# Kernel tuning notes

Measured on AMD Instinct MI355X. Metric: run time of the kernel, lower is better.

## Reference

```python
import jax, jax.numpy as jnp
import numpy as np

N_NODES = 20000
N_EDGES = 200000
D = 64            # node_encoding
H = 4             # num_heads
GRAPH_LAYERS = 2
FLOW_ITERS = 10


def seg_softmax(logits, seg, n):
    # numerically stable softmax over segments (per-row softmax of sparse matrix)
    m = jax.ops.segment_max(logits, seg, num_segments=n)
    e = jnp.exp(logits - m[seg])
    s = jax.ops.segment_sum(e, seg, num_segments=n)
    return e / s[seg]


def setup_inputs() -> dict:
    key = jax.random.key(0)
    ks = jax.random.split(key, 12)
    sc = 1.0 / np.sqrt(D)
    return {
        "node_embeddings": jax.random.normal(ks[0], (N_NODES, D), jnp.float32),
        "demands": jax.random.normal(ks[1], (N_NODES, 1), jnp.float32),
        "edge_row": jax.random.randint(ks[2], (N_EDGES,), 0, N_NODES, jnp.int32),
        "edge_col": jax.random.randint(ks[3], (N_EDGES,), 0, N_NODES, jnp.int32),
        "W_gat": jax.random.normal(ks[4], (H, D, D), jnp.float32) * sc,
        "a_src": jax.random.normal(ks[5], (H, D), jnp.float32) * sc,
        "a_dst": jax.random.normal(ks[6], (H, D), jnp.float32) * sc,
        "Wx": jax.random.normal(ks[7], (D, 3 * D), jnp.float32) * sc,
        "Wh": jax.random.normal(ks[8], (D, 3 * D), jnp.float32) * sc,
        "b_gru": jnp.zeros((3 * D,), jnp.float32),
        "Wd": jax.random.normal(ks[9], (D + 1, 1), jnp.float32) * sc,
        "bd": jnp.zeros((1,), jnp.float32),
    }


def reference(node_embeddings, demands, edge_row, edge_col,
              W_gat, a_src, a_dst, Wx, Wh, b_gru, Wd, bd):
    n = node_embeddings.shape[0]
    h = node_embeddings

    for _ in range(GRAPH_LAYERS):
        # ---- SparseGAT over adjacency edge list ----
        f = jnp.einsum('nd,hde->hne', h, W_gat)          # [H,N,D] per-head features
        s_src = jnp.einsum('hne,he->hn', f, a_src)       # [H,N]
        s_dst = jnp.einsum('hne,he->hn', f, a_dst)       # [H,N]
        logits = jax.nn.leaky_relu(s_src[:, edge_row] + s_dst[:, edge_col], 0.2)  # [H,E]
        alpha = jax.vmap(lambda l: seg_softmax(l, edge_row, n))(logits)           # [H,E]
        msgs = alpha[:, :, None] * f[:, edge_col, :]                              # [H,E,D]
        agg = jax.vmap(lambda m: jax.ops.segment_sum(m, edge_row, num_segments=n))(msgs)  # [H,N,D]
        gat_out = agg.mean(axis=0)                       # average heads -> [N,D]

        # ---- GRU node update (relu candidate activation), state = h ----
        xg = gat_out @ Wx + b_gru                        # [N,3D]
        z = jax.nn.sigmoid(xg[:, :D] + h @ Wh[:, :D])
        r = jax.nn.sigmoid(xg[:, D:2 * D] + h @ Wh[:, D:2 * D])
        hh = jax.nn.relu(xg[:, 2 * D:] + (r * h) @ Wh[:, 2 * D:])
        h = z * h + (1.0 - z) * hh

    # ---- decoder: linear over concat(encoding, demands) ----
    pred_w = jnp.concatenate([h, demands], axis=1) @ Wd + bd   # [N,1]

    # ---- sparse softmax of (adj * pred_weights) per source row ----
    w = seg_softmax(pred_w[edge_row, 0], edge_row, n)          # [E]

    # ---- iterative sparse MCF flow solve ----
    d_pos = jax.nn.relu(demands[:, 0])                         # source injections

    def step(flow, _):
        inflow = d_pos + jax.ops.segment_sum(flow, edge_col, num_segments=n)
        return w * inflow[edge_row], None

    flow, _ = jax.lax.scan(step, jnp.zeros_like(w), None, length=FLOW_ITERS)
    return flow
```

## Files before the change

### kernel.cpp

```cpp
#include <hip/hip_runtime.h>


#define N_NODES 20000
#define N_EDGES 200000
#define FLOW_ITERS 10
#define NBLK 128
#define NTHR 512
#define NPB 157
#define CAP 24
#define NQUAD 50000
#define QPB 391
#define OFL_MAX 4096
#define NP1 (N_NODES + 1)

__device__ __forceinline__ float ld_coh(const float* p) {
    return __hip_atomic_load(p, __ATOMIC_RELAXED, __HIP_MEMORY_SCOPE_AGENT);
}
__device__ __forceinline__ int ld_coh_i(const int* p) {
    return __hip_atomic_load(p, __ATOMIC_RELAXED, __HIP_MEMORY_SCOPE_AGENT);
}
__device__ __forceinline__ void st_coh(float* p, float v) {
    __hip_atomic_store(p, v, __ATOMIC_RELAXED, __HIP_MEMORY_SCOPE_AGENT);
}
__device__ __forceinline__ void st_coh_i(int* p, int v) {
    __hip_atomic_store(p, v, __ATOMIC_RELAXED, __HIP_MEMORY_SCOPE_AGENT);
}

__device__ __forceinline__ void gbar(int* grp, int ord) {
    __syncthreads();
    if (threadIdx.x == 0) {
        __hip_atomic_fetch_add(&grp[(blockIdx.x & 7) * 32], 1,
                               __ATOMIC_RELAXED, __HIP_MEMORY_SCOPE_AGENT);
        const int target = NBLK * ord;
        for (;;) {
            int s = 0;
            #pragma unroll
            for (int g = 0; g < 8; ++g)
                s += __hip_atomic_load(&grp[g * 32], __ATOMIC_RELAXED,
                                       __HIP_MEMORY_SCOPE_AGENT);
            if (s >= target) break;
            __builtin_amdgcn_s_sleep(1);
        }
    }
    __syncthreads();
}

__global__ __launch_bounds__(NTHR)
void mcf_fused(const float* __restrict__ demands,
               const int* __restrict__ edge_row,
               const int* __restrict__ edge_col,
               float* __restrict__ out,
               int* __restrict__ deg,
               int* __restrict__ fill,
               float* __restrict__ V0,
               float* __restrict__ V1b,
               int* __restrict__ pcsc,
               int* __restrict__ ofl_cnt,
               int* __restrict__ ofl_v,
               int* __restrict__ ofl_row,
               int* __restrict__ grp)
{
    const int tx = threadIdx.x, bx = blockIdx.x;
    int bar = 0;

    __shared__ float part[NTHR];

    const int m = bx * QPB + tx;
    const bool bld = (tx < QPB) && (m < NQUAD);
    int4 r4 = {0, 0, 0, 0}, c4 = {0, 0, 0, 0};
    if (bld) {
        r4 = ((const int4*)edge_row)[m];
        c4 = ((const int4*)edge_col)[m];
        int rr[4] = {r4.x, r4.y, r4.z, r4.w};
        int cc[4] = {c4.x, c4.y, c4.z, c4.w};
        #pragma unroll
        for (int i = 0; i < 4; ++i) {
            __hip_atomic_fetch_add(&deg[rr[i]], 1, __ATOMIC_RELAXED, __HIP_MEMORY_SCOPE_AGENT);
            int idx = __hip_atomic_fetch_add(&fill[cc[i]], 1,
                                             __ATOMIC_RELAXED, __HIP_MEMORY_SCOPE_AGENT);
            if (idx < CAP) {
                st_coh_i(&pcsc[cc[i] * CAP + idx], rr[i]);
            } else {
                int o = __hip_atomic_fetch_add(ofl_cnt, 1,
                                               __ATOMIC_RELAXED, __HIP_MEMORY_SCOPE_AGENT);
                if (o < OFL_MAX) { st_coh_i(&ofl_v[o], cc[i]); st_coh_i(&ofl_row[o], rr[i]); }
            }
        }
    }
    gbar(grp, ++bar);

    const int g = tx / 3, q = tx - 3 * g;
    const int v = bx * NPB + g;
    const bool active = (g < NPB) && (v < N_NODES);
    float dposv = 0.0f, invd = 0.0f;
    int   cnt = 0, ocnt = 0;
    int   er[8];
    if (active) {
        cnt = min(ld_coh_i(&fill[v]), CAP);
        const int4* pb = (const int4*)&pcsc[v * CAP + q * 8];
        int4 a = pb[0], b = pb[1];
        er[0]=a.x; er[1]=a.y; er[2]=a.z; er[3]=a.w;
        er[4]=b.x; er[5]=b.y; er[6]=b.z; er[7]=b.w;
        if (q == 0) {
            dposv  = fmaxf(demands[v], 0.0f);
            int dv = ld_coh_i(&deg[v]);
            invd   = (dv > 0) ? (1.0f / (float)dv) : 0.0f;
            ocnt   = ld_coh_i(ofl_cnt);
            st_coh(&V0[v], dposv * invd);
        }
    }
    gbar(grp, ++bar);

    #pragma unroll 1
    for (int j = 2; j <= FLOW_ITERS; ++j) {
        const float* Vp = (j & 1) ? V1b : V0;
        float*       Vn = (j & 1) ? V0 : V1b;
        if (active) {
            float p = 0.0f;
            #pragma unroll
            for (int s = 0; s < 8; ++s)
                if (q * 8 + s < cnt) p += ld_coh(&Vp[er[s]]);
            part[tx] = p;
        }
        __syncthreads();
        if (active && q == 0) {
            float acc = dposv + part[tx] + part[tx + 1] + part[tx + 2];
            if (ocnt > 0) {
                for (int o = 0; o < ocnt && o < OFL_MAX; ++o)
                    if (ld_coh_i(&ofl_v[o]) == v)
                        acc += ld_coh(&Vp[ld_coh_i(&ofl_row[o])]);
            }
            st_coh(&Vn[v], acc * invd);
        }
        gbar(grp, ++bar);
    }

    if (bld) {
        float4 o4;
        o4.x = ld_coh(&V1b[r4.x]);
        o4.y = ld_coh(&V1b[r4.y]);
        o4.z = ld_coh(&V1b[r4.z]);
        o4.w = ld_coh(&V1b[r4.w]);
        ((float4*)out)[m] = o4;
    }
}

extern "C" void kernel_launch(void* const* d_in, const int* in_sizes, int n_in,
                              void* d_out, int out_size, void* d_ws, size_t ws_size,
                              hipStream_t stream) {
    const float* demands  = (const float*)d_in[1];
    const int*   edge_row = (const int*)d_in[2];
    const int*   edge_col = (const int*)d_in[3];
    float*       out      = (float*)d_out;

    char* ws = (char*)d_ws;
    auto take = [&](size_t bytes) {
        void* p = (void*)ws;
        ws += (bytes + 127) & ~size_t(127);
        return p;
    };
    char* zone0 = ws;
    int*   deg     = (int*)  take(N_NODES * 4);
    int*   fill    = (int*)  take(N_NODES * 4);
    float* V0      = (float*)take(NP1 * 4);
    float* V1b     = (float*)take(NP1 * 4);
    int*   ofl_cnt = (int*)  take(4);
    int*   grp     = (int*)  take(8 * 32 * 4);
    size_t zone0_bytes = (size_t)(ws - zone0);
    int*   pcsc    = (int*)  take((size_t)N_NODES * CAP * 4);
    int*   ofl_v   = (int*)  take(OFL_MAX * 4);
    int*   ofl_row = (int*)  take(OFL_MAX * 4);

    hipMemsetAsync(zone0, 0x00, zone0_bytes, stream);
    mcf_fused<<<NBLK, NTHR, 0, stream>>>(demands, edge_row, edge_col, out,
                                         deg, fill, V0, V1b, pcsc,
                                         ofl_cnt, ofl_v, ofl_row, grp);
}
```

Baseline: 122.4 us.

## Replace per-iteration grid barriers with NaN-sentinel dataflow across level buffers

Removes the grid-wide barrier after each flow iteration. Each iteration level now gets its own buffer, pre-filled with a NaN bit pattern by a memset, and each node spins on its in-neighbours' entries until they are written, so waiting is point-to-point. It also computes the first level directly from demands and degrees, which saves one barrier, and assigns one thread per node instead of three. Risks include spin livelock if producers are not co-resident, reduced per-node parallelism, an extra memset, and a valid result that happens to equal the sentinel bit pattern.

Result: slower. 141.3 us (+15.4%).

```diff
diff --git a/kernel.cpp b/kernel.cpp
--- a/kernel.cpp
+++ b/kernel.cpp
@@ -12,8 +12,14 @@
 #define QPB 391
 #define OFL_MAX 4096
 #define NP1 (N_NODES + 1)
+#define NLVL 9
+#define NANP 0xFFFFFFFFu
+#define SPIN_MAX 65536
 
 __device__ __forceinline__ float ld_coh(const float* p) {
+    return __hip_atomic_load(p, __ATOMIC_RELAXED, __HIP_MEMORY_SCOPE_AGENT);
+}
+__device__ __forceinline__ unsigned ld_coh_u(const unsigned* p) {
     return __hip_atomic_load(p, __ATOMIC_RELAXED, __HIP_MEMORY_SCOPE_AGENT);
 }
 __device__ __forceinline__ int ld_coh_i(const int* p) {
@@ -32,7 +38,7 @@
         __hip_atomic_fetch_add(&grp[(blockIdx.x & 7) * 32], 1,
                                __ATOMIC_RELAXED, __HIP_MEMORY_SCOPE_AGENT);
         const int target = NBLK * ord;
-        for (;;) {
+        for (int t = 0; t < SPIN_MAX; ++t) {
             int s = 0;
             #pragma unroll
             for (int g = 0; g < 8; ++g)
@@ -52,8 +58,7 @@
                float* __restrict__ out,
                int* __restrict__ deg,
                int* __restrict__ fill,
-               float* __restrict__ V0,
-               float* __restrict__ V1b,
+               float* __restrict__ W,
                int* __restrict__ pcsc,
                int* __restrict__ ofl_cnt,
                int* __restrict__ ofl_v,
@@ -62,8 +67,6 @@
 {
     const int tx = threadIdx.x, bx = blockIdx.x;
     int bar = 0;
-
-    __shared__ float part[NTHR];
 
     const int m = bx * QPB + tx;
     const bool bld = (tx < QPB) && (m < NQUAD);
@@ -89,58 +92,94 @@
     }
     gbar(grp, ++bar);
 
-    const int g = tx / 3, q = tx - 3 * g;
-    const int v = bx * NPB + g;
-    const bool active = (g < NPB) && (v < N_NODES);
-    float dposv = 0.0f, invd = 0.0f;
-    int   cnt = 0, ocnt = 0;
-    int   er[8];
-    if (active) {
-        cnt = min(ld_coh_i(&fill[v]), CAP);
-        const int4* pb = (const int4*)&pcsc[v * CAP + q * 8];
-        int4 a = pb[0], b = pb[1];
-        er[0]=a.x; er[1]=a.y; er[2]=a.z; er[3]=a.w;
-        er[4]=b.x; er[5]=b.y; er[6]=b.z; er[7]=b.w;
-        if (q == 0) {
-            dposv  = fmaxf(demands[v], 0.0f);
-            int dv = ld_coh_i(&deg[v]);
-            invd   = (dv > 0) ? (1.0f / (float)dv) : 0.0f;
-            ocnt   = ld_coh_i(ofl_cnt);
-            st_coh(&V0[v], dposv * invd);
-        }
-    }
-    gbar(grp, ++bar);
-
-    #pragma unroll 1
-    for (int j = 2; j <= FLOW_ITERS; ++j) {
-        const float* Vp = (j & 1) ? V1b : V0;
-        float*       Vn = (j & 1) ? V0 : V1b;
-        if (active) {
-            float p = 0.0f;
-            #pragma unroll
-            for (int s = 0; s < 8; ++s)
-                if (q * 8 + s < cnt) p += ld_coh(&Vp[er[s]]);
-            part[tx] = p;
-        }
-        __syncthreads();
-        if (active && q == 0) {
-            float acc = dposv + part[tx] + part[tx + 1] + part[tx + 2];
+    const int v = bx * NPB + tx;
+    const bool own = (tx < NPB) && (v < N_NODES);
+    if (own) {
+        const int cnt = min(ld_coh_i(&fill[v]), CAP);
+        int er[CAP];
+        {
+            const int4* pb = (const int4*)&pcsc[v * CAP];
+            #pragma unroll
+            for (int qq = 0; qq < 6; ++qq) {
+                int4 a = pb[qq];
+                er[qq * 4 + 0] = a.x; er[qq * 4 + 1] = a.y;
+                er[qq * 4 + 2] = a.z; er[qq * 4 + 3] = a.w;
+            }
+        }
+        const float dposv = fmaxf(demands[v], 0.0f);
+        const int   dv    = ld_coh_i(&deg[v]);
+        const float invd  = (dv > 0) ? (1.0f / (float)dv) : 0.0f;
+        const int   ocnt  = ld_coh_i(ofl_cnt);
+
+        {
+            float fd[CAP]; int gd[CAP];
+            #pragma unroll
+            for (int s = 0; s < CAP; ++s)
+                if (s < cnt) { fd[s] = demands[er[s]]; gd[s] = ld_coh_i(&deg[er[s]]); }
+            float acc = dposv;
+            #pragma unroll
+            for (int s = 0; s < CAP; ++s)
+                if (s < cnt) acc += fmaxf(fd[s], 0.0f) * (1.0f / (float)gd[s]);
             if (ocnt > 0) {
                 for (int o = 0; o < ocnt && o < OFL_MAX; ++o)
-                    if (ld_coh_i(&ofl_v[o]) == v)
-                        acc += ld_coh(&Vp[ld_coh_i(&ofl_row[o])]);
-            }
-            st_coh(&Vn[v], acc * invd);
-        }
-        gbar(grp, ++bar);
-    }
+                    if (ld_coh_i(&ofl_v[o]) == v) {
+                        int r = ld_coh_i(&ofl_row[o]);
+                        acc += fmaxf(demands[r], 0.0f)
+                             * (1.0f / (float)ld_coh_i(&deg[r]));
+                    }
+            }
+            st_coh(&W[v], acc * invd);
+        }
+
+        #pragma unroll 1
+        for (int k = 1; k < NLVL; ++k) {
+            const float* Wp = W + (size_t)(k - 1) * NP1;
+            unsigned uv[CAP];
+            unsigned pend = (unsigned)((1ull << cnt) - 1ull);
+            int guard = 0;
+            while (pend) {
+                #pragma unroll
+                for (int s = 0; s < CAP; ++s)
+                    if ((pend >> s) & 1u)
+                        uv[s] = ld_coh_u((const unsigned*)&Wp[er[s]]);
+                unsigned np = pend;
+                #pragma unroll
+                for (int s = 0; s < CAP; ++s)
+                    if (((pend >> s) & 1u) && uv[s] != NANP) np &= ~(1u << s);
+                pend = np;
+                if (pend) {
+                    if (++guard > SPIN_MAX) break;
+                    __builtin_amdgcn_s_sleep(2);
+                }
+            }
+            float acc = dposv;
+            #pragma unroll
+            for (int s = 0; s < CAP; ++s)
+                if (s < cnt) acc += __uint_as_float(uv[s]);
+            if (ocnt > 0) {
+                for (int o = 0; o < ocnt && o < OFL_MAX; ++o)
+                    if (ld_coh_i(&ofl_v[o]) == v) {
+                        int r = ld_coh_i(&ofl_row[o]);
+                        unsigned u = NANP;
+                        for (int t = 0; t < SPIN_MAX; ++t) {
+                            u = ld_coh_u((const unsigned*)&Wp[r]);
+                            if (u != NANP) break;
+                        }
+                        acc += __uint_as_float(u);
+                    }
+            }
+            st_coh(&W[(size_t)k * NP1 + v], acc * invd);
+        }
+    }
+    gbar(grp, ++bar);
 
     if (bld) {
+        const float* W9 = W + (size_t)(NLVL - 1) * NP1;
         float4 o4;
-        o4.x = ld_coh(&V1b[r4.x]);
-        o4.y = ld_coh(&V1b[r4.y]);
-        o4.z = ld_coh(&V1b[r4.z]);
-        o4.w = ld_coh(&V1b[r4.w]);
+        o4.x = ld_coh(&W9[r4.x]);
+        o4.y = ld_coh(&W9[r4.y]);
+        o4.z = ld_coh(&W9[r4.z]);
+        o4.w = ld_coh(&W9[r4.w]);
         ((float4*)out)[m] = o4;
     }
 }
@@ -162,17 +201,19 @@
     char* zone0 = ws;
     int*   deg     = (int*)  take(N_NODES * 4);
     int*   fill    = (int*)  take(N_NODES * 4);
-    float* V0      = (float*)take(NP1 * 4);
-    float* V1b     = (float*)take(NP1 * 4);
     int*   ofl_cnt = (int*)  take(4);
     int*   grp     = (int*)  take(8 * 32 * 4);
     size_t zone0_bytes = (size_t)(ws - zone0);
+    char* zoneF = ws;
+    float* W       = (float*)take((size_t)NLVL * NP1 * 4);
+    size_t zoneF_bytes = (size_t)(ws - zoneF);
     int*   pcsc    = (int*)  take((size_t)N_NODES * CAP * 4);
     int*   ofl_v   = (int*)  take(OFL_MAX * 4);
     int*   ofl_row = (int*)  take(OFL_MAX * 4);
 
     hipMemsetAsync(zone0, 0x00, zone0_bytes, stream);
+    hipMemsetAsync(zoneF, 0xFF, zoneF_bytes, stream);
     mcf_fused<<<NBLK, NTHR, 0, stream>>>(demands, edge_row, edge_col, out,
-                                         deg, fill, V0, V1b, pcsc,
+                                         deg, fill, W, pcsc,
                                          ofl_cnt, ofl_v, ofl_row, grp);
 }
```

## Split build into separate kernel and run flow with one node per thread

Applied to the files above, without the earlier changes.

Moves the CSC build into its own launch so the kernel boundary replaces one grid barrier. The flow kernel now runs on 40 blocks with one thread per node holding all 24 neighbour indices in registers, which removes the shared-memory partial reduction and lets each barrier wait on fewer blocks. It also computes the second iteration directly from demands and degrees, saving one barrier round. The tradeoffs are an extra launch, higher register pressure, fewer CUs doing the gather, and a bounded spin in the barrier that could break correctness if it ever times out.

New measurement: 147.5 us. +20.5%, slower.

```diff
diff --git a/kernel.cpp b/kernel.cpp
--- a/kernel.cpp
+++ b/kernel.cpp
@@ -3,26 +3,20 @@
 
 #define N_NODES 20000
 #define N_EDGES 200000
-#define FLOW_ITERS 10
-#define NBLK 128
 #define NTHR 512
-#define NPB 157
+#define NBLK1 128
+#define QPB 391
+#define NBLK2 40
 #define CAP 24
 #define NQUAD 50000
-#define QPB 391
 #define OFL_MAX 4096
 #define NP1 (N_NODES + 1)
+#define SPIN_MAX 65536
 
 __device__ __forceinline__ float ld_coh(const float* p) {
     return __hip_atomic_load(p, __ATOMIC_RELAXED, __HIP_MEMORY_SCOPE_AGENT);
 }
-__device__ __forceinline__ int ld_coh_i(const int* p) {
-    return __hip_atomic_load(p, __ATOMIC_RELAXED, __HIP_MEMORY_SCOPE_AGENT);
-}
 __device__ __forceinline__ void st_coh(float* p, float v) {
-    __hip_atomic_store(p, v, __ATOMIC_RELAXED, __HIP_MEMORY_SCOPE_AGENT);
-}
-__device__ __forceinline__ void st_coh_i(int* p, int v) {
     __hip_atomic_store(p, v, __ATOMIC_RELAXED, __HIP_MEMORY_SCOPE_AGENT);
 }
 
@@ -31,8 +25,8 @@
     if (threadIdx.x == 0) {
         __hip_atomic_fetch_add(&grp[(blockIdx.x & 7) * 32], 1,
                                __ATOMIC_RELAXED, __HIP_MEMORY_SCOPE_AGENT);
-        const int target = NBLK * ord;
-        for (;;) {
+        const int target = NBLK2 * ord;
+        for (int t = 0; t < SPIN_MAX; ++t) {
             int s = 0;
             #pragma unroll
             for (int g = 0; g < 8; ++g)
@@ -46,102 +40,126 @@
 }
 
 __global__ __launch_bounds__(NTHR)
-void mcf_fused(const float* __restrict__ demands,
-               const int* __restrict__ edge_row,
-               const int* __restrict__ edge_col,
-               float* __restrict__ out,
-               int* __restrict__ deg,
-               int* __restrict__ fill,
-               float* __restrict__ V0,
-               float* __restrict__ V1b,
-               int* __restrict__ pcsc,
-               int* __restrict__ ofl_cnt,
-               int* __restrict__ ofl_v,
-               int* __restrict__ ofl_row,
-               int* __restrict__ grp)
+void build_k(const int* __restrict__ edge_row,
+             const int* __restrict__ edge_col,
+             int* __restrict__ deg,
+             int* __restrict__ fill,
+             int* __restrict__ pcsc,
+             int* __restrict__ ofl_cnt,
+             int* __restrict__ ofl_v,
+             int* __restrict__ ofl_row)
+{
+    const int m = blockIdx.x * QPB + threadIdx.x;
+    if (threadIdx.x < QPB && m < NQUAD) {
+        int4 r4 = ((const int4*)edge_row)[m];
+        int4 c4 = ((const int4*)edge_col)[m];
+        int rr[4] = {r4.x, r4.y, r4.z, r4.w};
+        int cc[4] = {c4.x, c4.y, c4.z, c4.w};
+        #pragma unroll
+        for (int i = 0; i < 4; ++i) {
+            __hip_atomic_fetch_add(&deg[rr[i]], 1,
+                                   __ATOMIC_RELAXED, __HIP_MEMORY_SCOPE_AGENT);
+            int idx = __hip_atomic_fetch_add(&fill[cc[i]], 1,
+                                             __ATOMIC_RELAXED, __HIP_MEMORY_SCOPE_AGENT);
+            if (idx < CAP) {
+                pcsc[cc[i] * CAP + idx] = rr[i];
+            } else {
+                int o = __hip_atomic_fetch_add(ofl_cnt, 1,
+                                               __ATOMIC_RELAXED, __HIP_MEMORY_SCOPE_AGENT);
+                if (o < OFL_MAX) { ofl_v[o] = cc[i]; ofl_row[o] = rr[i]; }
+            }
+        }
+    }
+}
+
+__global__ __launch_bounds__(NTHR)
+void flow_k(const float* __restrict__ demands,
+            const int* __restrict__ edge_row,
+            float* __restrict__ out,
+            const int* __restrict__ deg,
+            const int* __restrict__ fill,
+            const int* __restrict__ pcsc,
+            const int* __restrict__ ofl_cnt,
+            const int* __restrict__ ofl_v,
+            const int* __restrict__ ofl_row,
+            float* __restrict__ V0,
+            float* __restrict__ V1b,
+            int* __restrict__ grp)
 {
     const int tx = threadIdx.x, bx = blockIdx.x;
     int bar = 0;
 
-    __shared__ float part[NTHR];
-
-    const int m = bx * QPB + tx;
-    const bool bld = (tx < QPB) && (m < NQUAD);
-    int4 r4 = {0, 0, 0, 0}, c4 = {0, 0, 0, 0};
-    if (bld) {
-        r4 = ((const int4*)edge_row)[m];
-        c4 = ((const int4*)edge_col)[m];
-        int rr[4] = {r4.x, r4.y, r4.z, r4.w};
-        int cc[4] = {c4.x, c4.y, c4.z, c4.w};
-        #pragma unroll
-        for (int i = 0; i < 4; ++i) {
-            __hip_atomic_fetch_add(&deg[rr[i]], 1, __ATOMIC_RELAXED, __HIP_MEMORY_SCOPE_AGENT);
-            int idx = __hip_atomic_fetch_add(&fill[cc[i]], 1,
-                                             __ATOMIC_RELAXED, __HIP_MEMORY_SCOPE_AGENT);
-            if (idx < CAP) {
-                st_coh_i(&pcsc[cc[i] * CAP + idx], rr[i]);
-            } else {
-                int o = __hip_atomic_fetch_add(ofl_cnt, 1,
-                                               __ATOMIC_RELAXED, __HIP_MEMORY_SCOPE_AGENT);
-                if (o < OFL_MAX) { st_coh_i(&ofl_v[o], cc[i]); st_coh_i(&ofl_row[o], rr[i]); }
-            }
-        }
+    const int v = bx * NTHR + tx;
+    const bool own = (v < N_NODES);
+
+    int   er[CAP];
+    int   cnt = 0, ocnt = 0;
+    float dposv = 0.0f, invd = 0.0f;
+
+    if (own) {
+        cnt = min(fill[v], CAP);
+        const int4* pb = (const int4*)&pcsc[v * CAP];
+        #pragma unroll
+        for (int q = 0; q < 6; ++q) {
+            int4 a = pb[q];
+            er[q * 4 + 0] = a.x; er[q * 4 + 1] = a.y;
+            er[q * 4 + 2] = a.z; er[q * 4 + 3] = a.w;
+        }
+        const float dv_f = (float)deg[v];
+        dposv = fmaxf(demands[v], 0.0f);
+        invd  = (deg[v] > 0) ? (1.0f / dv_f) : 0.0f;
+        ocnt  = *ofl_cnt;
+
+        float acc = dposv;
+        #pragma unroll
+        for (int s = 0; s < CAP; ++s)
+            if (s < cnt)
+                acc += fmaxf(demands[er[s]], 0.0f) * (1.0f / (float)deg[er[s]]);
+        if (ocnt > 0) {
+            for (int o = 0; o < ocnt && o < OFL_MAX; ++o)
+                if (ofl_v[o] == v) {
+                    int r = ofl_row[o];
+                    acc += fmaxf(demands[r], 0.0f) * (1.0f / (float)deg[r]);
+                }
+        }
+        st_coh(&V0[v], acc * invd);
+
+        #pragma unroll
+        for (int s = 0; s < CAP; ++s)
+            if (s >= cnt) er[s] = N_NODES;
     }
     gbar(grp, ++bar);
 
-    const int g = tx / 3, q = tx - 3 * g;
-    const int v = bx * NPB + g;
-    const bool active = (g < NPB) && (v < N_NODES);
-    float dposv = 0.0f, invd = 0.0f;
-    int   cnt = 0, ocnt = 0;
-    int   er[8];
-    if (active) {
-        cnt = min(ld_coh_i(&fill[v]), CAP);
-        const int4* pb = (const int4*)&pcsc[v * CAP + q * 8];
-        int4 a = pb[0], b = pb[1];
-        er[0]=a.x; er[1]=a.y; er[2]=a.z; er[3]=a.w;
-        er[4]=b.x; er[5]=b.y; er[6]=b.z; er[7]=b.w;
-        if (q == 0) {
-            dposv  = fmaxf(demands[v], 0.0f);
-            int dv = ld_coh_i(&deg[v]);
-            invd   = (dv > 0) ? (1.0f / (float)dv) : 0.0f;
-            ocnt   = ld_coh_i(ofl_cnt);
-            st_coh(&V0[v], dposv * invd);
-        }
-    }
-    gbar(grp, ++bar);
-
     #pragma unroll 1
-    for (int j = 2; j <= FLOW_ITERS; ++j) {
-        const float* Vp = (j & 1) ? V1b : V0;
-        float*       Vn = (j & 1) ? V0 : V1b;
-        if (active) {
-            float p = 0.0f;
+    for (int j = 3; j <= 10; ++j) {
+        const float* Vp = (j & 1) ? V0 : V1b;
+        float*       Vn = (j & 1) ? V1b : V0;
+        if (own) {
+            float t[CAP];
             #pragma unroll
-            for (int s = 0; s < 8; ++s)
-                if (q * 8 + s < cnt) p += ld_coh(&Vp[er[s]]);
-            part[tx] = p;
-        }
-        __syncthreads();
-        if (active && q == 0) {
-            float acc = dposv + part[tx] + part[tx + 1] + part[tx + 2];
+            for (int s = 0; s < CAP; ++s)
+                t[s] = ld_coh(&Vp[er[s]]);
+            float acc = dposv;
+            #pragma unroll
+            for (int s = 0; s < CAP; ++s)
+                acc += t[s];
             if (ocnt > 0) {
                 for (int o = 0; o < ocnt && o < OFL_MAX; ++o)
-                    if (ld_coh_i(&ofl_v[o]) == v)
-                        acc += ld_coh(&Vp[ld_coh_i(&ofl_row[o])]);
+                    if (ofl_v[o] == v) acc += ld_coh(&Vp[ofl_row[o]]);
             }
             st_coh(&Vn[v], acc * invd);
         }
         gbar(grp, ++bar);
     }
 
-    if (bld) {
+    for (int qq = bx * NTHR + tx; qq < NQUAD; qq += NBLK2 * NTHR) {
+        int4 r4 = ((const int4*)edge_row)[qq];
         float4 o4;
-        o4.x = ld_coh(&V1b[r4.x]);
-        o4.y = ld_coh(&V1b[r4.y]);
-        o4.z = ld_coh(&V1b[r4.z]);
-        o4.w = ld_coh(&V1b[r4.w]);
-        ((float4*)out)[m] = o4;
+        o4.x = ld_coh(&V0[r4.x]);
+        o4.y = ld_coh(&V0[r4.y]);
+        o4.z = ld_coh(&V0[r4.z]);
+        o4.w = ld_coh(&V0[r4.w]);
+        ((float4*)out)[qq] = o4;
     }
 }
 
@@ -172,7 +190,11 @@
     int*   ofl_row = (int*)  take(OFL_MAX * 4);
 
     hipMemsetAsync(zone0, 0x00, zone0_bytes, stream);
-    mcf_fused<<<NBLK, NTHR, 0, stream>>>(demands, edge_row, edge_col, out,
-                                         deg, fill, V0, V1b, pcsc,
-                                         ofl_cnt, ofl_v, ofl_row, grp);
-}
+    build_k<<<NBLK1, NTHR, 0, stream>>>(edge_row, edge_col,
+                                        deg, fill, pcsc,
+                                        ofl_cnt, ofl_v, ofl_row);
+    flow_k<<<NBLK2, NTHR, 0, stream>>>(demands, edge_row, out,
+                                       deg, fill, pcsc,
+                                       ofl_cnt, ofl_v, ofl_row,
+                                       V0, V1b, grp);
+}
```

## Fold first flow iteration into setup phase and relax coherent loads with fences

Applied to the files above, without the earlier changes.

Computes the second flow iterate directly from demands and degrees during the CSC-read phase, which removes one grid-wide barrier and one propagation round. Plain stores and loads replace the agent-scope atomic ones for the CSC build data, with release and acquire fences around the first barrier. The barrier counters are spread over 16 cache lines instead of 8 to reduce contention. The spin loop is now capped, which bounds a hang but could let a block proceed early if the barrier is very slow.

Result: slower. 158.0 us (+29.1%).

```diff
diff --git a/kernel.cpp b/kernel.cpp
--- a/kernel.cpp
+++ b/kernel.cpp
@@ -3,7 +3,6 @@
 
 #define N_NODES 20000
 #define N_EDGES 200000
-#define FLOW_ITERS 10
 #define NBLK 128
 #define NTHR 512
 #define NPB 157
@@ -12,30 +11,32 @@
 #define QPB 391
 #define OFL_MAX 4096
 #define NP1 (N_NODES + 1)
+#define SPIN_MAX 65536
+#define NLINE 16
 
 __device__ __forceinline__ float ld_coh(const float* p) {
-    return __hip_atomic_load(p, __ATOMIC_RELAXED, __HIP_MEMORY_SCOPE_AGENT);
-}
-__device__ __forceinline__ int ld_coh_i(const int* p) {
     return __hip_atomic_load(p, __ATOMIC_RELAXED, __HIP_MEMORY_SCOPE_AGENT);
 }
 __device__ __forceinline__ void st_coh(float* p, float v) {
     __hip_atomic_store(p, v, __ATOMIC_RELAXED, __HIP_MEMORY_SCOPE_AGENT);
 }
-__device__ __forceinline__ void st_coh_i(int* p, int v) {
-    __hip_atomic_store(p, v, __ATOMIC_RELAXED, __HIP_MEMORY_SCOPE_AGENT);
+__device__ __forceinline__ void acq_fence() {
+    __builtin_amdgcn_fence(__ATOMIC_ACQUIRE, "agent");
+}
+__device__ __forceinline__ void rel_fence() {
+    __builtin_amdgcn_fence(__ATOMIC_RELEASE, "agent");
 }
 
 __device__ __forceinline__ void gbar(int* grp, int ord) {
     __syncthreads();
     if (threadIdx.x == 0) {
-        __hip_atomic_fetch_add(&grp[(blockIdx.x & 7) * 32], 1,
+        __hip_atomic_fetch_add(&grp[(blockIdx.x & (NLINE - 1)) * 32], 1,
                                __ATOMIC_RELAXED, __HIP_MEMORY_SCOPE_AGENT);
         const int target = NBLK * ord;
-        for (;;) {
+        for (int t = 0; t < SPIN_MAX; ++t) {
             int s = 0;
             #pragma unroll
-            for (int g = 0; g < 8; ++g)
+            for (int g = 0; g < NLINE; ++g)
                 s += __hip_atomic_load(&grp[g * 32], __ATOMIC_RELAXED,
                                        __HIP_MEMORY_SCOPE_AGENT);
             if (s >= target) break;
@@ -67,27 +68,30 @@
 
     const int m = bx * QPB + tx;
     const bool bld = (tx < QPB) && (m < NQUAD);
-    int4 r4 = {0, 0, 0, 0}, c4 = {0, 0, 0, 0};
+    int4 r4 = {0, 0, 0, 0};
     if (bld) {
         r4 = ((const int4*)edge_row)[m];
-        c4 = ((const int4*)edge_col)[m];
+        int4 c4 = ((const int4*)edge_col)[m];
         int rr[4] = {r4.x, r4.y, r4.z, r4.w};
         int cc[4] = {c4.x, c4.y, c4.z, c4.w};
         #pragma unroll
         for (int i = 0; i < 4; ++i) {
-            __hip_atomic_fetch_add(&deg[rr[i]], 1, __ATOMIC_RELAXED, __HIP_MEMORY_SCOPE_AGENT);
+            __hip_atomic_fetch_add(&deg[rr[i]], 1,
+                                   __ATOMIC_RELAXED, __HIP_MEMORY_SCOPE_AGENT);
             int idx = __hip_atomic_fetch_add(&fill[cc[i]], 1,
                                              __ATOMIC_RELAXED, __HIP_MEMORY_SCOPE_AGENT);
             if (idx < CAP) {
-                st_coh_i(&pcsc[cc[i] * CAP + idx], rr[i]);
+                pcsc[cc[i] * CAP + idx] = rr[i];
             } else {
                 int o = __hip_atomic_fetch_add(ofl_cnt, 1,
                                                __ATOMIC_RELAXED, __HIP_MEMORY_SCOPE_AGENT);
-                if (o < OFL_MAX) { st_coh_i(&ofl_v[o], cc[i]); st_coh_i(&ofl_row[o], rr[i]); }
+                if (o < OFL_MAX) { ofl_v[o] = cc[i]; ofl_row[o] = rr[i]; }
             }
         }
     }
+    rel_fence();
     gbar(grp, ++bar);
+    acq_fence();
 
     const int g = tx / 3, q = tx - 3 * g;
     const int v = bx * NPB + g;
@@ -96,25 +100,42 @@
     int   cnt = 0, ocnt = 0;
     int   er[8];
     if (active) {
-        cnt = min(ld_coh_i(&fill[v]), CAP);
+        cnt = min(fill[v], CAP);
         const int4* pb = (const int4*)&pcsc[v * CAP + q * 8];
         int4 a = pb[0], b = pb[1];
         er[0]=a.x; er[1]=a.y; er[2]=a.z; er[3]=a.w;
         er[4]=b.x; er[5]=b.y; er[6]=b.z; er[7]=b.w;
         if (q == 0) {
             dposv  = fmaxf(demands[v], 0.0f);
-            int dv = ld_coh_i(&deg[v]);
+            int dv = deg[v];
             invd   = (dv > 0) ? (1.0f / (float)dv) : 0.0f;
-            ocnt   = ld_coh_i(ofl_cnt);
-            st_coh(&V0[v], dposv * invd);
+            ocnt   = *ofl_cnt;
         }
+        float p = 0.0f;
+        #pragma unroll
+        for (int s = 0; s < 8; ++s)
+            if (q * 8 + s < cnt)
+                p += fmaxf(demands[er[s]], 0.0f) * (1.0f / (float)deg[er[s]]);
+        part[tx] = p;
+    }
+    __syncthreads();
+    if (active && q == 0) {
+        float acc = dposv + part[tx] + part[tx + 1] + part[tx + 2];
+        if (ocnt > 0) {
+            for (int o = 0; o < ocnt && o < OFL_MAX; ++o)
+                if (ofl_v[o] == v) {
+                    int r = ofl_row[o];
+                    acc += fmaxf(demands[r], 0.0f) * (1.0f / (float)deg[r]);
+                }
+        }
+        st_coh(&V0[v], acc * invd);
     }
     gbar(grp, ++bar);
 
     #pragma unroll 1
-    for (int j = 2; j <= FLOW_ITERS; ++j) {
-        const float* Vp = (j & 1) ? V1b : V0;
-        float*       Vn = (j & 1) ? V0 : V1b;
+    for (int j = 3; j <= 10; ++j) {
+        const float* Vp = (j & 1) ? V0 : V1b;
+        float*       Vn = (j & 1) ? V1b : V0;
         if (active) {
             float p = 0.0f;
             #pragma unroll
@@ -127,8 +148,7 @@
             float acc = dposv + part[tx] + part[tx + 1] + part[tx + 2];
             if (ocnt > 0) {
                 for (int o = 0; o < ocnt && o < OFL_MAX; ++o)
-                    if (ld_coh_i(&ofl_v[o]) == v)
-                        acc += ld_coh(&Vp[ld_coh_i(&ofl_row[o])]);
+                    if (ofl_v[o] == v) acc += ld_coh(&Vp[ofl_row[o]]);
             }
             st_coh(&Vn[v], acc * invd);
         }
@@ -137,10 +157,10 @@
 
     if (bld) {
         float4 o4;
-        o4.x = ld_coh(&V1b[r4.x]);
-        o4.y = ld_coh(&V1b[r4.y]);
-        o4.z = ld_coh(&V1b[r4.z]);
-        o4.w = ld_coh(&V1b[r4.w]);
+        o4.x = ld_coh(&V0[r4.x]);
+        o4.y = ld_coh(&V0[r4.y]);
+        o4.z = ld_coh(&V0[r4.z]);
+        o4.w = ld_coh(&V0[r4.w]);
         ((float4*)out)[m] = o4;
     }
 }
@@ -165,7 +185,7 @@
     float* V0      = (float*)take(NP1 * 4);
     float* V1b     = (float*)take(NP1 * 4);
     int*   ofl_cnt = (int*)  take(4);
-    int*   grp     = (int*)  take(8 * 32 * 4);
+    int*   grp     = (int*)  take(NLINE * 32 * 4);
     size_t zone0_bytes = (size_t)(ws - zone0);
     int*   pcsc    = (int*)  take((size_t)N_NODES * CAP * 4);
     int*   ofl_v   = (int*)  take(OFL_MAX * 4);
```
